# Kernel optimization log

Measured on AMD Instinct MI355X. Metric: run time of the kernel, lower is better.

Reference implementation:

```python
import jax, jax.numpy as jnp
import numpy as np

# Dimensions (Llama-3-8B-style GQA with paged KV cache)
B, S, HID = 1, 1024, 4096
H, HKV, D = 32, 8, 128
G = H // HKV
BLK = 16            # tokens per KV block
NB = 256            # blocks in storage
CB = 192            # context blocks attended (3072 tokens)
PAST = 2048         # tokens already cached before this step
NL = 2              # layers in kv_ptr
L = CB * BLK


def rotate_half(x):
    x1, x2 = x[..., : x.shape[-1] // 2], x[..., x.shape[-1] // 2:]
    return jnp.concatenate([-x2, x1], axis=-1)


def setup_inputs() -> dict:
    key = jax.random.key(0)
    ks = jax.random.split(key, 8)
    hidden_states = jax.random.normal(ks[0], (B, S, HID), jnp.float32)
    kv_ptr = jax.random.normal(ks[1], (NL, 2, NB, HKV, BLK, D), jnp.float32)
    Wq = 0.02 * jax.random.normal(ks[2], (H * D, HID), jnp.float32)
    Wk = 0.02 * jax.random.normal(ks[3], (HKV * D, HID), jnp.float32)
    Wv = 0.02 * jax.random.normal(ks[4], (HKV * D, HID), jnp.float32)
    Wo = 0.02 * jax.random.normal(ks[5], (HID, H * D), jnp.float32)
    # RoPE cache for the new tokens (global positions PAST..PAST+S-1), HF convention
    pos = (PAST + jnp.arange(S)).astype(jnp.float32)
    inv_freq = 1.0 / (10000.0 ** (jnp.arange(0, D, 2, dtype=jnp.float32) / D))
    freqs = pos[:, None] * inv_freq[None, :]                # [S, D/2]
    emb = jnp.concatenate([freqs, freqs], axis=-1)           # [S, D]
    cos = jnp.cos(emb)[None, None]                           # [1,1,S,D]
    sin = jnp.sin(emb)[None, None]
    new_q_lut = jnp.arange(S, dtype=jnp.int32)[None]         # identity query LUT
    new_kv_lut = (CB - S // BLK + jnp.arange(S // BLK, dtype=jnp.int32))[None]  # blocks 128..191
    all_kv_lut = jnp.arange(CB, dtype=jnp.int32)[None]       # blocks 0..191
    kv_pos = jnp.arange(L)
    q_pos = PAST + jnp.arange(S)
    mask = (kv_pos[None, None, :] <= q_pos[None, :, None])   # [1,S,L] causal over global positions
    cmd_groups = jnp.zeros((B, S), jnp.int32)                # split-K scheduling metadata (no math effect)
    return dict(hidden_states=hidden_states, kv_ptr=kv_ptr, new_q_lut=new_q_lut,
                new_kv_lut=new_kv_lut, all_kv_lut=all_kv_lut, mask=mask,
                cmd_groups=cmd_groups, cos=cos, sin=sin, Wq=Wq, Wk=Wk, Wv=Wv, Wo=Wo,
                layer_idx=0)


def reference(hidden_states, kv_ptr, new_q_lut, new_kv_lut, all_kv_lut, mask,
              cmd_groups, cos, sin, Wq, Wk, Wv, Wo, layer_idx):
    b, s, _ = hidden_states.shape
    # QKV projections (no bias)
    q = jnp.einsum('bsh,oh->bso', hidden_states, Wq).reshape(b, s, H, D).transpose(0, 2, 1, 3)
    k = jnp.einsum('bsh,oh->bso', hidden_states, Wk).reshape(b, s, HKV, D).transpose(0, 2, 1, 3)
    v = jnp.einsum('bsh,oh->bso', hidden_states, Wv).reshape(b, s, HKV, D).transpose(0, 2, 1, 3)
    # RoPE
    q = q * cos + rotate_half(q) * sin
    k = k * cos + rotate_half(k) * sin
    # fill_kv_block_storage: scatter new K/V blocks into this layer's storage (b == 1)
    kb = jnp.transpose(k[0].reshape(HKV, s // BLK, BLK, D), (1, 0, 2, 3))  # [nblk,HKV,BLK,D]
    vb = jnp.transpose(v[0].reshape(HKV, s // BLK, BLK, D), (1, 0, 2, 3))
    sk = kv_ptr[layer_idx, 0].at[new_kv_lut[0]].set(kb)
    sv = kv_ptr[layer_idx, 1].at[new_kv_lut[0]].set(vb)
    # qkv_attention: gather context blocks via LUT, masked GQA attention
    ck = jnp.transpose(sk[all_kv_lut[0]], (1, 0, 2, 3)).reshape(HKV, L, D)  # [HKV,L,D]
    cv = jnp.transpose(sv[all_kv_lut[0]], (1, 0, 2, 3)).reshape(HKV, L, D)
    qg = q[:, :, new_q_lut[0], :].reshape(b, HKV, G, s, D)
    scores = jnp.einsum('bkgsd,kld->bkgsl', qg, ck) / jnp.sqrt(jnp.float32(D))
    scores = jnp.where(mask[:, None, None], scores, jnp.finfo(scores.dtype).min)
    p = jax.nn.softmax(scores, axis=-1)
    o = jnp.einsum('bkgsl,kld->bkgsd', p, cv).reshape(b, H, s, D)
    o = o.transpose(0, 2, 1, 3).reshape(b, s, H * D)
    return jnp.einsum('bso,ho->bsh', o, Wo)
```

## Files before the change

### kernel.cpp

```cpp
#include <hip/hip_runtime.h>
#include <cstdint>
#include <cstddef>


typedef _Float16 f16;
typedef f16 f16x8 __attribute__((ext_vector_type(8)));
typedef f16 f16x4 __attribute__((ext_vector_type(4)));
typedef float f32x4 __attribute__((ext_vector_type(4)));

#define HIDN 4096
#define LCTX 3072
#define PASTN 2048
#define QK_SCALE_LOG2 0.12753102734366334f
#define RESC_THR 11.54f

__device__ __forceinline__ f32x4 mfma16(f16x8 a, f16x8 b, f32x4 c) {
    return __builtin_amdgcn_mfma_f32_16x16x32_f16(a, b, c, 0, 0, 0);
}
__device__ __forceinline__ f32x4 mfma16k16(f16x4 a, f16x4 b, f32x4 c) {
    return __builtin_amdgcn_mfma_f32_16x16x16f16(a, b, c, 0, 0, 0);
}

__device__ __forceinline__ void gl_lds16(const void* g, void* l) {
    auto gp = (const __attribute__((address_space(1))) unsigned int*)(uintptr_t)g;
    auto lp = (__attribute__((address_space(3))) unsigned int*)(uintptr_t)l;
    __builtin_amdgcn_global_load_lds(gp, lp, 16, 0, 0);
}

__device__ __forceinline__ uint32_t lds_lo(const void* p) {
    return (uint32_t)(uintptr_t)p;
}

#define TRRD(dst, va, OFF) \
    asm volatile("ds_read_b64_tr_b16 %0, %1 offset:" #OFF : "=v"(dst) : "v"(va))
#define WAITL(N) \
    asm volatile("s_waitcnt lgkmcnt(" #N ")" ::: "memory"); \
    __builtin_amdgcn_sched_barrier(0)

__global__ void cvt_all(const float* __restrict__ hidden, const float* __restrict__ Wq,
                        const float* __restrict__ Wk, const float* __restrict__ Wv,
                        f16* __restrict__ h16, f16* __restrict__ w16)
{
    int i = blockIdx.x * 256 + threadIdx.x;
    const float* src; f16* dst; int off;
    if (i < 1048576)      { src = hidden; dst = h16; off = i; }
    else if (i < 5242880) { src = Wq; dst = w16; off = i - 1048576; }
    else if (i < 6291456) { src = Wk; dst = w16 + (size_t)4096 * 4096; off = i - 5242880; }
    else                  { src = Wv; dst = w16 + (size_t)5120 * 4096; off = i - 6291456; }
    f32x4 v = *(const f32x4*)(src + (size_t)off * 4);
    f16x4 h;
#pragma unroll
    for (int j = 0; j < 4; j++) h[j] = (f16)v[j];
    *(f16x4*)(dst + (size_t)off * 4) = h;
}

template <int EPI>
__global__ __launch_bounds__(256, 3) void gemm_f16(
    const f16* __restrict__ A, const f16* __restrict__ B,
    float* __restrict__ Cf, f16* __restrict__ Cq, f16* __restrict__ Ck,
    f16* __restrict__ Cv, int M, int N, int K)
{
    __shared__ f16 As[128 * 64];
    __shared__ f16 Bs[128 * 64];

    const int t = threadIdx.x, lane = t & 63, w = t >> 6;
    const int wm = w >> 1, wn = w & 1;
    const int l16 = lane & 15, g16 = lane >> 4;
    const int m0 = blockIdx.y * 128, n0 = blockIdx.x * 128;

    const int srow = lane >> 3;
    const int sgr  = (lane & 7) ^ srow;

    const size_t aoff = (size_t)(m0 + w * 32 + srow) * K + sgr * 8;
    const size_t boff = (size_t)(n0 + w * 32 + srow) * K + sgr * 8;

    f32x4 acc[4][4];
#pragma unroll
    for (int i = 0; i < 4; i++)
#pragma unroll
        for (int j = 0; j < 4; j++) acc[i][j] = (f32x4){0.f, 0.f, 0.f, 0.f};

    for (int k0 = 0; k0 < K; k0 += 64) {
#pragma unroll
        for (int j = 0; j < 4; j++) {
            gl_lds16(A + aoff + (size_t)j * 8 * K + k0, (void*)(As + (w * 32 + j * 8) * 64));
            gl_lds16(B + boff + (size_t)j * 8 * K + k0, (void*)(Bs + (w * 32 + j * 8) * 64));
        }
        __syncthreads();

#pragma unroll
        for (int ks = 0; ks < 2; ks++) {
            f16x8 af[4], bfr[4];
#pragma unroll
            for (int mi = 0; mi < 4; mi++) {
                int r = wm * 64 + mi * 16 + l16;
                int g = ks * 4 + g16;
                af[mi] = *(const f16x8*)&As[r * 64 + ((g ^ (r & 7)) << 3)];
            }
#pragma unroll
            for (int ni = 0; ni < 4; ni++) {
                int r = wn * 64 + ni * 16 + l16;
                int g = ks * 4 + g16;
                bfr[ni] = *(const f16x8*)&Bs[r * 64 + ((g ^ (r & 7)) << 3)];
            }
#pragma unroll
            for (int ni = 0; ni < 4; ni++)
#pragma unroll
                for (int mi = 0; mi < 4; mi++)
                    acc[mi][ni] = mfma16(af[mi], bfr[ni], acc[mi][ni]);
        }
        __syncthreads();
    }

#pragma unroll
    for (int mi = 0; mi < 4; mi++)
#pragma unroll
        for (int ni = 0; ni < 4; ni++)
#pragma unroll
            for (int r = 0; r < 4; r++) {
                int row = m0 + wm * 64 + mi * 16 + (g16 << 2) + r;
                int col = n0 + wn * 64 + ni * 16 + l16;
                float val = acc[mi][ni][r];
                if (EPI == 0) {
                    if (col < 4096) {
                        Cq[(size_t)row * 4096 + col] = (f16)val;
                    } else if (col < 5120) {
                        Ck[(size_t)row * 1024 + (col - 4096)] = (f16)val;
                    } else {
                        int c = col - 5120;
                        int hh = c >> 7, d = c & 127;
                        Cv[((size_t)hh * LCTX + PASTN + row) * 128 + d] = (f16)val;
                    }
                } else {
                    Cf[(size_t)row * N + col] = val;
                }
            }
}

__global__ void aux_all(const float* __restrict__ Wo, f16* __restrict__ w16,
                        f16* __restrict__ q16, const f16* __restrict__ kraw,
                        const float* __restrict__ cosp, const float* __restrict__ sinp,
                        f16* __restrict__ ck, const float* __restrict__ kvp,
                        const int* __restrict__ layer, f16* __restrict__ cv)
{
    int i = blockIdx.x * 256 + threadIdx.x;
    if (i < 4194304) {
        f32x4 v = *(const f32x4*)(Wo + (size_t)i * 4);
        f16x4 h;
#pragma unroll
        for (int j = 0; j < 4; j++) h[j] = (f16)v[j];
        *(f16x4*)(w16 + (size_t)i * 4) = h;
    } else if (i < 4456448) {
        int ii = i - 4194304;
        int gd = ii & 7, hh = (ii >> 3) & 31, s = ii >> 8;
        size_t b1 = (size_t)s * 4096 + hh * 128 + gd * 8;
        f16x8 x1 = *(f16x8*)(q16 + b1);
        f16x8 x2 = *(f16x8*)(q16 + b1 + 64);
        const float* c1 = cosp + s * 128 + gd * 8;
        const float* s1 = sinp + s * 128 + gd * 8;
        f16x8 o1, o2;
#pragma unroll
        for (int j = 0; j < 8; j++) {
            float a = (float)x1[j], b = (float)x2[j];
            o1[j] = (f16)((a * c1[j] - b * s1[j]) * QK_SCALE_LOG2);
            o2[j] = (f16)((b * c1[j + 64] + a * s1[j + 64]) * QK_SCALE_LOG2);
        }
        *(f16x8*)(q16 + b1) = o1;
        *(f16x8*)(q16 + b1 + 64) = o2;
    } else if (i < 4521984) {
        int ii = i - 4456448;
        int gd = ii & 7, kvh = (ii >> 3) & 7, s = ii >> 6;
        size_t b1 = (size_t)s * 1024 + kvh * 128 + gd * 8;
        f16x8 x1 = *(const f16x8*)(kraw + b1);
        f16x8 x2 = *(const f16x8*)(kraw + b1 + 64);
        const float* c1 = cosp + s * 128 + gd * 8;
        const float* s1 = sinp + s * 128 + gd * 8;
        f16x8 o1, o2;
#pragma unroll
        for (int j = 0; j < 8; j++) {
            float a = (float)x1[j], b = (float)x2[j];
            o1[j] = (f16)(a * c1[j] - b * s1[j]);
            o2[j] = (f16)(b * c1[j + 64] + a * s1[j + 64]);
        }
        size_t dst = ((size_t)kvh * LCTX + PASTN + s) * 128 + gd * 8;
        *(f16x8*)(ck + dst) = o1;
        *(f16x8*)(ck + dst + 64) = o2;
    } else {
        int i4 = i - 4521984;
        int half = i4 >> 19;
        int e = (i4 & 524287) * 4;
        int hh = e >> 18, rem = e & 262143, l = rem >> 7, d = rem & 127;
        int blk = l >> 4, rr = l & 15;
        size_t src = (((size_t)(layer[0] * 2 + half) * 256 + blk) * 8 + hh) * 2048
                   + (size_t)rr * 128 + d;
        f32x4 x = *(const f32x4*)(kvp + src);
        f16x4 h;
#pragma unroll
        for (int j = 0; j < 4; j++) h[j] = (f16)x[j];
        size_t dst = ((size_t)hh * LCTX + l) * 128 + d;
        *(f16x4*)((half ? cv : ck) + dst) = h;
    }
}

__global__ __launch_bounds__(256, 2) void attn_part(
    const f16* __restrict__ Q, const f16* __restrict__ Kc,
    const f16* __restrict__ Vc, f16* __restrict__ Op, float* __restrict__ mlb)
{
    const int b = blockIdx.x;
    const int z = b >> 8;
    const int idx = b & 255;
    const int h = idx & 31;
    const int jj = idx >> 5;
    const int j = z ? (7 - jj) : jj;
    const int s0 = j * 128;
    const int kvh = h >> 2;
    const int t = threadIdx.x, lane = t & 63, w = t >> 6;
    const int l16 = lane & 15, g16 = lane >> 4;

    __shared__ f16 Ks[2][64 * 128];
    __shared__ f16 Vs[2][64 * 128];

    f16x8 qfA[4], qfB[4];
    {
        size_t baseA = (size_t)(s0 + w * 32 + l16) * 4096 + h * 128;
        size_t baseB = baseA + (size_t)16 * 4096;
#pragma unroll
        for (int kk = 0; kk < 4; kk++) {
            qfA[kk] = *(const f16x8*)(Q + baseA + kk * 32 + g16 * 8);
            qfB[kk] = *(const f16x8*)(Q + baseB + kk * 32 + g16 * 8);
        }
    }

    f32x4 ofA[8], ofB[8];
#pragma unroll
    for (int cf = 0; cf < 8; cf++) {
        ofA[cf] = (f32x4){0.f, 0.f, 0.f, 0.f};
        ofB[cf] = (f32x4){0.f, 0.f, 0.f, 0.f};
    }
    float mrA = -3.0e38f, lrA = 0.f;
    float mrB = -3.0e38f, lrB = 0.f;

    const f16* Kb = Kc + (size_t)kvh * LCTX * 128;
    const f16* Vb = Vc + (size_t)kvh * LCTX * 128;
    const int ntt = (PASTN + s0 + 128) >> 6;

    const int krow = lane >> 4;
    const int kp   = lane & 15;
    const int vrow = ((lane >> 5) << 4) + (((lane >> 3) & 3) << 2) + ((lane >> 1) & 3);
    const int vch  = (lane & 1) << 3;

    const uint32_t vs0 = lds_lo(Vs[0]) + lane * 8;
    const uint32_t vs1 = lds_lo(Vs[1]) + lane * 8;

#define STAGE_KV(l0, buf)                                                     \
    {                                                                         \
        _Pragma("unroll")                                                     \
        for (int jx = 0; jx < 4; jx++) {                                      \
            int r7 = ((jx & 1) << 2) + krow;                                  \
            int sg = kp ^ r7;                                                 \
            gl_lds16(Kb + (size_t)((l0) + w * 16 + jx * 4 + krow) * 128 + sg * 8, \
                     (void*)(Ks[buf] + (w * 16 + jx * 4) * 128));             \
        }                                                                     \
        _Pragma("unroll")                                                     \
        for (int q = 0; q < 4; q++) {                                         \
            gl_lds16(Vb + (size_t)((l0) + (q & 1) * 32 + vrow) * 128          \
                        + (w * 2 + (q >> 1)) * 16 + vch,                      \
                     (void*)(Vs[buf] + (w * 4 + q) * 512));                   \
        }                                                                     \
    }

    STAGE_KV(z * 64, 0);
    __syncthreads();

    int itp = 0;
    for (int it = z; it < ntt; it += 2, ++itp) {
        const int l0 = it << 6;
        const int cur = itp & 1;

        if (it + 2 < ntt) STAGE_KV(l0 + 128, cur ^ 1);

        f32x4 sA[4], sB[4];
#pragma unroll
        for (int ni = 0; ni < 4; ni++) {
            sA[ni] = (f32x4){0.f, 0.f, 0.f, 0.f};
            sB[ni] = (f32x4){0.f, 0.f, 0.f, 0.f};
        }
        __builtin_amdgcn_s_setprio(1);
#pragma unroll
        for (int ni = 0; ni < 4; ni++)
#pragma unroll
            for (int kk = 0; kk < 4; kk++) {
                int r = ni * 16 + l16;
                int g = kk * 4 + g16;
                f16x8 kh = *(const f16x8*)&Ks[cur][r * 128 + ((g ^ (r & 7)) << 3)];
                sA[ni] = mfma16(kh, qfA[kk], sA[ni]);
                sB[ni] = mfma16(kh, qfB[kk], sB[ni]);
            }
        __builtin_amdgcn_s_setprio(0);

#define SOFTMAX(sf, mr, lr, of, QOFF)                                          \
        {                                                                      \
            const int qrow = s0 + w * 32 + (QOFF) + l16;                       \
            if (l0 + 63 > PASTN + s0 + w * 32 + (QOFF)) {                      \
                _Pragma("unroll")                                              \
                for (int ni = 0; ni < 4; ni++)                                 \
                    _Pragma("unroll")                                          \
                    for (int r = 0; r < 4; r++) {                              \
                        int col = l0 + ni * 16 + (g16 << 2) + r;               \
                        if (col > PASTN + qrow) sf[ni][r] = -3.0e38f;          \
                    }                                                          \
            }                                                                  \
            float mx;                                                          \
            {                                                                  \
                f32x4 m4 = sf[0];                                              \
                _Pragma("unroll")                                              \
                for (int ni = 1; ni < 4; ni++) {                               \
                    m4[0] = fmaxf(m4[0], sf[ni][0]);                           \
                    m4[1] = fmaxf(m4[1], sf[ni][1]);                           \
                    m4[2] = fmaxf(m4[2], sf[ni][2]);                           \
                    m4[3] = fmaxf(m4[3], sf[ni][3]);                           \
                }                                                              \
                mx = fmaxf(fmaxf(m4[0], m4[1]), fmaxf(m4[2], m4[3]));          \
            }                                                                  \
            mx = fmaxf(mx, __shfl_xor(mx, 16));                                \
            mx = fmaxf(mx, __shfl_xor(mx, 32));                                \
            if (__any(mx > mr + RESC_THR)) {                                   \
                float mnew = fmaxf(mr, mx);                                    \
                float corr = exp2f(mr - mnew);                                 \
                mr = mnew;                                                     \
                lr *= corr;                                                    \
                float cr[4];                                                   \
                _Pragma("unroll")                                              \
                for (int r = 0; r < 4; r++) cr[r] = __shfl(corr, (g16 << 2) + r); \
                _Pragma("unroll")                                              \
                for (int cf = 0; cf < 8; cf++)                                 \
                    _Pragma("unroll")                                          \
                    for (int r = 0; r < 4; r++) of[cf][r] *= cr[r];            \
            }                                                                  \
            _Pragma("unroll")                                                  \
            for (int ni = 0; ni < 4; ni++)                                     \
                _Pragma("unroll")                                              \
                for (int r = 0; r < 4; r++) {                                  \
                    float p = exp2f(sf[ni][r] - mr);                           \
                    sf[ni][r] = p;                                             \
                    lr += p;                                                   \
                }                                                              \
        }

        SOFTMAX(sA, mrA, lrA, ofA, 0)
        SOFTMAX(sB, mrB, lrB, ofB, 16)

        f16x4 paA[4], paB[4];
#pragma unroll
        for (int ni = 0; ni < 4; ni++) {
            paA[ni][0] = (f16)sA[ni][0]; paA[ni][1] = (f16)sA[ni][1];
            paA[ni][2] = (f16)sA[ni][2]; paA[ni][3] = (f16)sA[ni][3];
            paB[ni][0] = (f16)sB[ni][0]; paB[ni][1] = (f16)sB[ni][1];
            paB[ni][2] = (f16)sB[ni][2]; paB[ni][3] = (f16)sB[ni][3];
        }

        {
            const uint32_t va = cur ? vs1 : vs0;
            f16x4 ra0, ra1, ra2, ra3, rb0, rb1, rb2, rb3;
            f16x4 rc0, rc1, rc2, rc3, rd0, rd1, rd2, rd3;
            __builtin_amdgcn_s_setprio(1);
            TRRD(ra0,va,0);     TRRD(ra1,va,512);   TRRD(ra2,va,1024);  TRRD(ra3,va,1536);
            TRRD(rb0,va,2048);  TRRD(rb1,va,2560);  TRRD(rb2,va,3072);  TRRD(rb3,va,3584);
            TRRD(rc0,va,4096);  TRRD(rc1,va,4608);  TRRD(rc2,va,5120);  TRRD(rc3,va,5632);
#define X2(cf, ni, reg) \
            ofA[cf] = mfma16k16(paA[ni], reg, ofA[cf]); \
            ofB[cf] = mfma16k16(paB[ni], reg, ofB[cf]);
            WAITL(8);
            X2(0,0,ra0) X2(0,1,ra1) X2(0,2,ra2) X2(0,3,ra3)
            TRRD(rd0,va,6144);  TRRD(rd1,va,6656);  TRRD(rd2,va,7168);  TRRD(rd3,va,7680);
            WAITL(8);
            X2(1,0,rb0) X2(1,1,rb1) X2(1,2,rb2) X2(1,3,rb3)
            TRRD(ra0,va,8192);  TRRD(ra1,va,8704);  TRRD(ra2,va,9216);  TRRD(ra3,va,9728);
            WAITL(8);
            X2(2,0,rc0) X2(2,1,rc1) X2(2,2,rc2) X2(2,3,rc3)
            TRRD(rb0,va,10240); TRRD(rb1,va,10752); TRRD(rb2,va,11264); TRRD(rb3,va,11776);
            WAITL(8);
            X2(3,0,rd0) X2(3,1,rd1) X2(3,2,rd2) X2(3,3,rd3)
            TRRD(rc0,va,12288); TRRD(rc1,va,12800); TRRD(rc2,va,13312); TRRD(rc3,va,13824);
            WAITL(8);
            X2(4,0,ra0) X2(4,1,ra1) X2(4,2,ra2) X2(4,3,ra3)
            TRRD(rd0,va,14336); TRRD(rd1,va,14848); TRRD(rd2,va,15360); TRRD(rd3,va,15872);
            WAITL(8);
            X2(5,0,rb0) X2(5,1,rb1) X2(5,2,rb2) X2(5,3,rb3)
            WAITL(4);
            X2(6,0,rc0) X2(6,1,rc1) X2(6,2,rc2) X2(6,3,rc3)
            WAITL(0);
            X2(7,0,rd0) X2(7,1,rd1) X2(7,2,rd2) X2(7,3,rd3)
#undef X2
            __builtin_amdgcn_s_setprio(0);
        }
        __syncthreads();
    }

#define WRITE_P(of, mr, lr, QOFF)                                             \
    {                                                                         \
        float l2 = lr + __shfl_xor(lr, 16);                                   \
        l2 += __shfl_xor(l2, 32);                                             \
        if (lane < 16) {                                                      \
            int srow = s0 + w * 32 + (QOFF) + lane;                           \
            *(float2*)(mlb + (((size_t)z * 1024 + srow) * 32 + h) * 2) =      \
                make_float2(mr, l2);                                          \
        }                                                                     \
        float lrr[4];                                                         \
        _Pragma("unroll")                                                     \
        for (int r = 0; r < 4; r++) lrr[r] = __shfl(l2, (g16 << 2) + r);      \
        _Pragma("unroll")                                                     \
        for (int cf = 0; cf < 8; cf++)                                        \
            _Pragma("unroll")                                                 \
            for (int r = 0; r < 4; r++) {                                     \
                int srow = s0 + w * 32 + (QOFF) + (g16 << 2) + r;             \
                int d = cf * 16 + l16;                                        \
                Op[(size_t)z * 4194304 + (size_t)srow * 4096                  \
                   + (size_t)h * 128 + d] = (f16)(of[cf][r] / lrr[r]);        \
            }                                                                 \
    }
    WRITE_P(ofA, mrA, lrA, 0)
    WRITE_P(ofB, mrB, lrB, 16)
#undef WRITE_P
#undef SOFTMAX
#undef STAGE_KV
}

__global__ void attn_combine(const f16* __restrict__ Op, const float* __restrict__ mlb,
                             f16* __restrict__ obuf)
{
    int i = blockIdx.x * 256 + threadIdx.x;
    int d8 = i & 15, hh = (i >> 4) & 31, s = i >> 9;
    float2 ml0 = *(const float2*)(mlb + (((size_t)0 * 1024 + s) * 32 + hh) * 2);
    float2 ml1 = *(const float2*)(mlb + (((size_t)1 * 1024 + s) * 32 + hh) * 2);
    float mstar = fmaxf(ml0.x, ml1.x);
    float w0 = exp2f(ml0.x - mstar) * ml0.y;
    float w1 = exp2f(ml1.x - mstar) * ml1.y;
    float inv = 1.0f / (w0 + w1);
    size_t off = (size_t)s * 4096 + (size_t)hh * 128 + d8 * 8;
    f16x8 a = *(const f16x8*)(Op + off);
    f16x8 b = *(const f16x8*)(Op + 4194304 + off);
    f16x8 o;
#pragma unroll
    for (int jx = 0; jx < 8; jx++)
        o[jx] = (f16)(((float)a[jx] * w0 + (float)b[jx] * w1) * inv);
    *(f16x8*)(obuf + off) = o;
}

extern "C" void kernel_launch(void* const* d_in, const int* in_sizes, int n_in,
                              void* d_out, int out_size, void* d_ws, size_t ws_size,
                              hipStream_t stream)
{
    const float* hidden = (const float*)d_in[0];
    const float* kvp    = (const float*)d_in[1];
    const float* cosp   = (const float*)d_in[7];
    const float* sinp   = (const float*)d_in[8];
    const float* Wq     = (const float*)d_in[9];
    const float* Wk     = (const float*)d_in[10];
    const float* Wv     = (const float*)d_in[11];
    const float* Wo     = (const float*)d_in[12];
    const int*   layer  = (const int*)d_in[13];

    char* ws = (char*)d_ws;
    f16* w16  = (f16*)ws;
    f16* opart= (f16*)(ws + 33554432);
    f16* h16  = (f16*)(ws + 50331648);
    f16* ck   = (f16*)(ws + 58720256);
    f16* cv   = (f16*)(ws + 65011712);
    f16* obuf = (f16*)(ws + 71303168);

    f16*   q16  = (f16*)d_out;
    f16*   kraw = (f16*)((char*)d_out + 8388608);
    float* mlb  = (float*)((char*)d_out + 8388608);

    cvt_all<<<28672, 256, 0, stream>>>(hidden, Wq, Wk, Wv, h16, w16);

    gemm_f16<0><<<dim3(48, 8), 256, 0, stream>>>(
        h16, w16, nullptr, q16, kraw, cv, 1024, 6144, 4096);

    aux_all<<<21760, 256, 0, stream>>>(Wo, w16, q16, kraw, cosp, sinp,
                                       ck, kvp, layer, cv);

    attn_part<<<dim3(512), 256, 0, stream>>>(q16, ck, cv, opart, mlb);

    attn_combine<<<2048, 256, 0, stream>>>(opart, mlb, obuf);

    gemm_f16<1><<<dim3(32, 8), 256, 0, stream>>>(
        obuf, w16, (float*)d_out, nullptr, nullptr, nullptr, 1024, 4096, 4096);
}
```

Measured before the change: 272.2 us.

## Fold KV-cache conversion into QKV GEMM blocks and compute softmax row sums via MFMA

The fp32-to-fp16 conversion of the cached K/V context moves out of the aux kernel into 256 extra blocks of the QKV GEMM launch (now a 1D grid), so it runs alongside the GEMM tiles. The attention kernel now accumulates softmax denominators with an extra MFMA against a ones vector instead of scalar adds and cross-lane shuffles. The m and l statistics are stored in separate arrays. Tradeoffs: extra MFMA work per tile, and the copy blocks compete with GEMM blocks for CUs. Row sums now come from fp16-rounded probabilities.

```diff
diff --git a/kernel.cpp b/kernel.cpp
--- a/kernel.cpp
+++ b/kernel.cpp
@@ -58,15 +58,42 @@
 __global__ __launch_bounds__(256, 3) void gemm_f16(
     const f16* __restrict__ A, const f16* __restrict__ B,
     float* __restrict__ Cf, f16* __restrict__ Cq, f16* __restrict__ Ck,
-    f16* __restrict__ Cv, int M, int N, int K)
+    f16* __restrict__ Cv, int M, int N, int K,
+    const float* __restrict__ kvp, const int* __restrict__ layer,
+    f16* __restrict__ ckc)
 {
     __shared__ f16 As[128 * 64];
     __shared__ f16 Bs[128 * 64];
 
+    const int bx = blockIdx.x;
+
+    if (EPI == 0 && bx >= 384) {
+        const int lay = layer[0];
+        int base = (bx - 384) * 256 + threadIdx.x;
+#pragma unroll
+        for (int pass = 0; pass < 16; ++pass) {
+            int i4 = base + pass * 65536;
+            int half = i4 >> 19;
+            int e = (i4 & 524287) * 4;
+            int hh = e >> 18, rem = e & 262143, l = rem >> 7, d = rem & 127;
+            int blk = l >> 4, rr = l & 15;
+            size_t src = (((size_t)(lay * 2 + half) * 256 + blk) * 8 + hh) * 2048
+                       + (size_t)rr * 128 + d;
+            f32x4 x = *(const f32x4*)(kvp + src);
+            f16x4 h;
+#pragma unroll
+            for (int j = 0; j < 4; j++) h[j] = (f16)x[j];
+            size_t dst = ((size_t)hh * LCTX + l) * 128 + d;
+            *(f16x4*)((half ? Cv : ckc) + dst) = h;
+        }
+        return;
+    }
+
     const int t = threadIdx.x, lane = t & 63, w = t >> 6;
     const int wm = w >> 1, wn = w & 1;
     const int l16 = lane & 15, g16 = lane >> 4;
-    const int m0 = blockIdx.y * 128, n0 = blockIdx.x * 128;
+    const int nx = (EPI == 0) ? 48 : 32;
+    const int m0 = (bx / nx) * 128, n0 = (bx % nx) * 128;
 
     const int srow = lane >> 3;
     const int sgr  = (lane & 7) ^ srow;
@@ -137,11 +164,10 @@
             }
 }
 
-__global__ void aux_all(const float* __restrict__ Wo, f16* __restrict__ w16,
-                        f16* __restrict__ q16, const f16* __restrict__ kraw,
-                        const float* __restrict__ cosp, const float* __restrict__ sinp,
-                        f16* __restrict__ ck, const float* __restrict__ kvp,
-                        const int* __restrict__ layer, f16* __restrict__ cv)
+__global__ void aux2(const float* __restrict__ Wo, f16* __restrict__ w16,
+                     f16* __restrict__ q16, const f16* __restrict__ kraw,
+                     const float* __restrict__ cosp, const float* __restrict__ sinp,
+                     f16* __restrict__ ck)
 {
     int i = blockIdx.x * 256 + threadIdx.x;
     if (i < 4194304) {
@@ -167,7 +193,7 @@
         }
         *(f16x8*)(q16 + b1) = o1;
         *(f16x8*)(q16 + b1 + 64) = o2;
-    } else if (i < 4521984) {
+    } else {
         int ii = i - 4456448;
         int gd = ii & 7, kvh = (ii >> 3) & 7, s = ii >> 6;
         size_t b1 = (size_t)s * 1024 + kvh * 128 + gd * 8;
@@ -185,26 +211,13 @@
         size_t dst = ((size_t)kvh * LCTX + PASTN + s) * 128 + gd * 8;
         *(f16x8*)(ck + dst) = o1;
         *(f16x8*)(ck + dst + 64) = o2;
-    } else {
-        int i4 = i - 4521984;
-        int half = i4 >> 19;
-        int e = (i4 & 524287) * 4;
-        int hh = e >> 18, rem = e & 262143, l = rem >> 7, d = rem & 127;
-        int blk = l >> 4, rr = l & 15;
-        size_t src = (((size_t)(layer[0] * 2 + half) * 256 + blk) * 8 + hh) * 2048
-                   + (size_t)rr * 128 + d;
-        f32x4 x = *(const f32x4*)(kvp + src);
-        f16x4 h;
-#pragma unroll
-        for (int j = 0; j < 4; j++) h[j] = (f16)x[j];
-        size_t dst = ((size_t)hh * LCTX + l) * 128 + d;
-        *(f16x4*)((half ? cv : ck) + dst) = h;
     }
 }
 
 __global__ __launch_bounds__(256, 2) void attn_part(
     const f16* __restrict__ Q, const f16* __restrict__ Kc,
-    const f16* __restrict__ Vc, f16* __restrict__ Op, float* __restrict__ mlb)
+    const f16* __restrict__ Vc, f16* __restrict__ Op,
+    float* __restrict__ mlb_m, float* __restrict__ mlb_l)
 {
     const int b = blockIdx.x;
     const int z = b >> 8;
@@ -237,8 +250,10 @@
         ofA[cf] = (f32x4){0.f, 0.f, 0.f, 0.f};
         ofB[cf] = (f32x4){0.f, 0.f, 0.f, 0.f};
     }
-    float mrA = -3.0e38f, lrA = 0.f;
-    float mrB = -3.0e38f, lrB = 0.f;
+    f32x4 lsA = (f32x4){0.f, 0.f, 0.f, 0.f};
+    f32x4 lsB = (f32x4){0.f, 0.f, 0.f, 0.f};
+    float mrA = -3.0e38f, mrB = -3.0e38f;
+    const f16x4 vone = {(f16)1.f, (f16)1.f, (f16)1.f, (f16)1.f};
 
     const f16* Kb = Kc + (size_t)kvh * LCTX * 128;
     const f16* Vb = Vc + (size_t)kvh * LCTX * 128;
@@ -298,7 +313,7 @@
             }
         __builtin_amdgcn_s_setprio(0);
 
-#define SOFTMAX(sf, mr, lr, of, QOFF)                                          \
+#define SOFTMAX(sf, mr, ls, of, QOFF)                                          \
         {                                                                      \
             const int qrow = s0 + w * 32 + (QOFF) + l16;                       \
             if (l0 + 63 > PASTN + s0 + w * 32 + (QOFF)) {                      \
@@ -328,10 +343,11 @@
                 float mnew = fmaxf(mr, mx);                                    \
                 float corr = exp2f(mr - mnew);                                 \
                 mr = mnew;                                                     \
-                lr *= corr;                                                    \
                 float cr[4];                                                   \
                 _Pragma("unroll")                                              \
                 for (int r = 0; r < 4; r++) cr[r] = __shfl(corr, (g16 << 2) + r); \
+                _Pragma("unroll")                                              \
+                for (int r = 0; r < 4; r++) ls[r] *= cr[r];                    \
                 _Pragma("unroll")                                              \
                 for (int cf = 0; cf < 8; cf++)                                 \
                     _Pragma("unroll")                                          \
@@ -340,15 +356,12 @@
             _Pragma("unroll")                                                  \
             for (int ni = 0; ni < 4; ni++)                                     \
                 _Pragma("unroll")                                              \
-                for (int r = 0; r < 4; r++) {                                  \
-                    float p = exp2f(sf[ni][r] - mr);                           \
-                    sf[ni][r] = p;                                             \
-                    lr += p;                                                   \
-                }                                                              \
-        }
-
-        SOFTMAX(sA, mrA, lrA, ofA, 0)
-        SOFTMAX(sB, mrB, lrB, ofB, 16)
+                for (int r = 0; r < 4; r++)                                    \
+                    sf[ni][r] = exp2f(sf[ni][r] - mr);                         \
+        }
+
+        SOFTMAX(sA, mrA, lsA, ofA, 0)
+        SOFTMAX(sB, mrB, lsB, ofB, 16)
 
         f16x4 paA[4], paB[4];
 #pragma unroll
@@ -367,6 +380,11 @@
             TRRD(ra0,va,0);     TRRD(ra1,va,512);   TRRD(ra2,va,1024);  TRRD(ra3,va,1536);
             TRRD(rb0,va,2048);  TRRD(rb1,va,2560);  TRRD(rb2,va,3072);  TRRD(rb3,va,3584);
             TRRD(rc0,va,4096);  TRRD(rc1,va,4608);  TRRD(rc2,va,5120);  TRRD(rc3,va,5632);
+#pragma unroll
+            for (int ni = 0; ni < 4; ni++) {
+                lsA = mfma16k16(paA[ni], vone, lsA);
+                lsB = mfma16k16(paB[ni], vone, lsB);
+            }
 #define X2(cf, ni, reg) \
             ofA[cf] = mfma16k16(paA[ni], reg, ofA[cf]); \
             ofB[cf] = mfma16k16(paB[ni], reg, ofB[cf]);
@@ -397,18 +415,19 @@
         __syncthreads();
     }
 
-#define WRITE_P(of, mr, lr, QOFF)                                             \
+#define WRITE_P(of, mr, ls, QOFF)                                             \
     {                                                                         \
-        float l2 = lr + __shfl_xor(lr, 16);                                   \
-        l2 += __shfl_xor(l2, 32);                                             \
         if (lane < 16) {                                                      \
             int srow = s0 + w * 32 + (QOFF) + lane;                           \
-            *(float2*)(mlb + (((size_t)z * 1024 + srow) * 32 + h) * 2) =      \
-                make_float2(mr, l2);                                          \
+            mlb_m[((size_t)z * 1024 + srow) * 32 + h] = mr;                   \
         }                                                                     \
-        float lrr[4];                                                         \
-        _Pragma("unroll")                                                     \
-        for (int r = 0; r < 4; r++) lrr[r] = __shfl(l2, (g16 << 2) + r);      \
+        if (l16 == 0) {                                                       \
+            _Pragma("unroll")                                                 \
+            for (int r = 0; r < 4; r++) {                                     \
+                int srow = s0 + w * 32 + (QOFF) + (g16 << 2) + r;             \
+                mlb_l[((size_t)z * 1024 + srow) * 32 + h] = ls[r];            \
+            }                                                                 \
+        }                                                                     \
         _Pragma("unroll")                                                     \
         for (int cf = 0; cf < 8; cf++)                                        \
             _Pragma("unroll")                                                 \
@@ -416,26 +435,30 @@
                 int srow = s0 + w * 32 + (QOFF) + (g16 << 2) + r;             \
                 int d = cf * 16 + l16;                                        \
                 Op[(size_t)z * 4194304 + (size_t)srow * 4096                  \
-                   + (size_t)h * 128 + d] = (f16)(of[cf][r] / lrr[r]);        \
+                   + (size_t)h * 128 + d] = (f16)(of[cf][r] / ls[r]);         \
             }                                                                 \
     }
-    WRITE_P(ofA, mrA, lrA, 0)
-    WRITE_P(ofB, mrB, lrB, 16)
+    WRITE_P(ofA, mrA, lsA, 0)
+    WRITE_P(ofB, mrB, lsB, 16)
 #undef WRITE_P
 #undef SOFTMAX
 #undef STAGE_KV
 }
 
-__global__ void attn_combine(const f16* __restrict__ Op, const float* __restrict__ mlb,
+__global__ void attn_combine(const f16* __restrict__ Op,
+                             const float* __restrict__ mlb_m,
+                             const float* __restrict__ mlb_l,
                              f16* __restrict__ obuf)
 {
     int i = blockIdx.x * 256 + threadIdx.x;
     int d8 = i & 15, hh = (i >> 4) & 31, s = i >> 9;
-    float2 ml0 = *(const float2*)(mlb + (((size_t)0 * 1024 + s) * 32 + hh) * 2);
-    float2 ml1 = *(const float2*)(mlb + (((size_t)1 * 1024 + s) * 32 + hh) * 2);
-    float mstar = fmaxf(ml0.x, ml1.x);
-    float w0 = exp2f(ml0.x - mstar) * ml0.y;
-    float w1 = exp2f(ml1.x - mstar) * ml1.y;
+    float m0 = mlb_m[(size_t)s * 32 + hh];
+    float m1 = mlb_m[(size_t)(1024 + s) * 32 + hh];
+    float l0 = mlb_l[(size_t)s * 32 + hh];
+    float l1 = mlb_l[(size_t)(1024 + s) * 32 + hh];
+    float mstar = fmaxf(m0, m1);
+    float w0 = exp2f(m0 - mstar) * l0;
+    float w1 = exp2f(m1 - mstar) * l1;
     float inv = 1.0f / (w0 + w1);
     size_t off = (size_t)s * 4096 + (size_t)hh * 128 + d8 * 8;
     f16x8 a = *(const f16x8*)(Op + off);
@@ -469,22 +492,23 @@
     f16* cv   = (f16*)(ws + 65011712);
     f16* obuf = (f16*)(ws + 71303168);
 
-    f16*   q16  = (f16*)d_out;
-    f16*   kraw = (f16*)((char*)d_out + 8388608);
-    float* mlb  = (float*)((char*)d_out + 8388608);
+    f16*   q16   = (f16*)d_out;
+    f16*   kraw  = (f16*)((char*)d_out + 8388608);
+    float* mlb_m = (float*)((char*)d_out + 8388608);
+    float* mlb_l = (float*)((char*)d_out + 8650752);
 
     cvt_all<<<28672, 256, 0, stream>>>(hidden, Wq, Wk, Wv, h16, w16);
 
-    gemm_f16<0><<<dim3(48, 8), 256, 0, stream>>>(
-        h16, w16, nullptr, q16, kraw, cv, 1024, 6144, 4096);
-
-    aux_all<<<21760, 256, 0, stream>>>(Wo, w16, q16, kraw, cosp, sinp,
-                                       ck, kvp, layer, cv);
-
-    attn_part<<<dim3(512), 256, 0, stream>>>(q16, ck, cv, opart, mlb);
-
-    attn_combine<<<2048, 256, 0, stream>>>(opart, mlb, obuf);
-
-    gemm_f16<1><<<dim3(32, 8), 256, 0, stream>>>(
-        obuf, w16, (float*)d_out, nullptr, nullptr, nullptr, 1024, 4096, 4096);
-}
+    gemm_f16<0><<<dim3(640), 256, 0, stream>>>(
+        h16, w16, nullptr, q16, kraw, cv, 1024, 6144, 4096, kvp, layer, ck);
+
+    aux2<<<17664, 256, 0, stream>>>(Wo, w16, q16, kraw, cosp, sinp, ck);
+
+    attn_part<<<dim3(512), 256, 0, stream>>>(q16, ck, cv, opart, mlb_m, mlb_l);
+
+    attn_combine<<<2048, 256, 0, stream>>>(opart, mlb_m, mlb_l, obuf);
+
+    gemm_f16<1><<<dim3(256), 256, 0, stream>>>(
+        obuf, w16, (float*)d_out, nullptr, nullptr, nullptr, 1024, 4096, 4096,
+        nullptr, nullptr, nullptr);
+}
```

Result: no change. 275.3 us (+1.1%).

## Fold KV cache conversion into QKV GEMM tail blocks; halve O-proj tile height

Applied to the files above, without the earlier changes.

The QKV projection GEMM now launches 512 blocks on a 1D grid. The first 384 compute GEMM tiles and the last 128 convert the cached fp32 K/V blocks to fp16, a job taken out of the aux kernel. This lets the memory-bound cache conversion overlap with the compute-bound GEMM instead of running as a separate phase. The output projection GEMM is templated to a 64-row tile, doubling its block count to 512 so more CUs are filled, at the cost of less reuse per tile.

```diff
diff --git a/kernel.cpp b/kernel.cpp
--- a/kernel.cpp
+++ b/kernel.cpp
@@ -54,46 +54,79 @@
     *(f16x4*)(dst + (size_t)off * 4) = h;
 }
 
-template <int EPI>
+template <int EPI, int BM>
 __global__ __launch_bounds__(256, 3) void gemm_f16(
     const f16* __restrict__ A, const f16* __restrict__ B,
     float* __restrict__ Cf, f16* __restrict__ Cq, f16* __restrict__ Ck,
-    f16* __restrict__ Cv, int M, int N, int K)
+    f16* __restrict__ Cv, int M, int N, int K,
+    const float* __restrict__ kvp, const int* __restrict__ layer,
+    f16* __restrict__ ckc)
 {
-    __shared__ f16 As[128 * 64];
+    __shared__ f16 As[BM * 64];
     __shared__ f16 Bs[128 * 64];
+
+    const int bx = blockIdx.x;
+
+    if (EPI == 0 && bx >= 384) {
+        const int lay = layer[0];
+        int base = (bx - 384) * 256 + threadIdx.x;
+#pragma unroll
+        for (int pass = 0; pass < 32; ++pass) {
+            int i4 = base + pass * 32768;
+            int half = i4 >> 19;
+            int e = (i4 & 524287) * 4;
+            int hh = e >> 18, rem = e & 262143, l = rem >> 7, d = rem & 127;
+            int blk = l >> 4, rr = l & 15;
+            size_t src = (((size_t)(lay * 2 + half) * 256 + blk) * 8 + hh) * 2048
+                       + (size_t)rr * 128 + d;
+            f32x4 x = *(const f32x4*)(kvp + src);
+            f16x4 h;
+#pragma unroll
+            for (int j = 0; j < 4; j++) h[j] = (f16)x[j];
+            size_t dst = ((size_t)hh * LCTX + l) * 128 + d;
+            *(f16x4*)((half ? Cv : ckc) + dst) = h;
+        }
+        return;
+    }
+
+    constexpr int RPW = BM / 4;
+    constexpr int MI  = BM / 32;
 
     const int t = threadIdx.x, lane = t & 63, w = t >> 6;
     const int wm = w >> 1, wn = w & 1;
     const int l16 = lane & 15, g16 = lane >> 4;
-    const int m0 = blockIdx.y * 128, n0 = blockIdx.x * 128;
+    const int nx = (EPI == 0) ? 48 : 32;
+    const int m0 = (bx / nx) * BM, n0 = (bx % nx) * 128;
 
     const int srow = lane >> 3;
     const int sgr  = (lane & 7) ^ srow;
 
-    const size_t aoff = (size_t)(m0 + w * 32 + srow) * K + sgr * 8;
+    const size_t aoff = (size_t)(m0 + w * RPW + srow) * K + sgr * 8;
     const size_t boff = (size_t)(n0 + w * 32 + srow) * K + sgr * 8;
 
-    f32x4 acc[4][4];
-#pragma unroll
-    for (int i = 0; i < 4; i++)
+    f32x4 acc[MI][4];
+#pragma unroll
+    for (int i = 0; i < MI; i++)
 #pragma unroll
         for (int j = 0; j < 4; j++) acc[i][j] = (f32x4){0.f, 0.f, 0.f, 0.f};
 
     for (int k0 = 0; k0 < K; k0 += 64) {
 #pragma unroll
-        for (int j = 0; j < 4; j++) {
-            gl_lds16(A + aoff + (size_t)j * 8 * K + k0, (void*)(As + (w * 32 + j * 8) * 64));
-            gl_lds16(B + boff + (size_t)j * 8 * K + k0, (void*)(Bs + (w * 32 + j * 8) * 64));
-        }
+        for (int j = 0; j < RPW / 8; j++)
+            gl_lds16(A + aoff + (size_t)j * 8 * K + k0,
+                     (void*)(As + (w * RPW + j * 8) * 64));
+#pragma unroll
+        for (int j = 0; j < 4; j++)
+            gl_lds16(B + boff + (size_t)j * 8 * K + k0,
+                     (void*)(Bs + (w * 32 + j * 8) * 64));
         __syncthreads();
 
 #pragma unroll
         for (int ks = 0; ks < 2; ks++) {
-            f16x8 af[4], bfr[4];
-#pragma unroll
-            for (int mi = 0; mi < 4; mi++) {
-                int r = wm * 64 + mi * 16 + l16;
+            f16x8 af[MI], bfr[4];
+#pragma unroll
+            for (int mi = 0; mi < MI; mi++) {
+                int r = wm * (BM / 2) + mi * 16 + l16;
                 int g = ks * 4 + g16;
                 af[mi] = *(const f16x8*)&As[r * 64 + ((g ^ (r & 7)) << 3)];
             }
@@ -106,19 +139,19 @@
 #pragma unroll
             for (int ni = 0; ni < 4; ni++)
 #pragma unroll
-                for (int mi = 0; mi < 4; mi++)
+                for (int mi = 0; mi < MI; mi++)
                     acc[mi][ni] = mfma16(af[mi], bfr[ni], acc[mi][ni]);
         }
         __syncthreads();
     }
 
 #pragma unroll
-    for (int mi = 0; mi < 4; mi++)
+    for (int mi = 0; mi < MI; mi++)
 #pragma unroll
         for (int ni = 0; ni < 4; ni++)
 #pragma unroll
             for (int r = 0; r < 4; r++) {
-                int row = m0 + wm * 64 + mi * 16 + (g16 << 2) + r;
+                int row = m0 + wm * (BM / 2) + mi * 16 + (g16 << 2) + r;
                 int col = n0 + wn * 64 + ni * 16 + l16;
                 float val = acc[mi][ni][r];
                 if (EPI == 0) {
@@ -137,11 +170,10 @@
             }
 }
 
-__global__ void aux_all(const float* __restrict__ Wo, f16* __restrict__ w16,
-                        f16* __restrict__ q16, const f16* __restrict__ kraw,
-                        const float* __restrict__ cosp, const float* __restrict__ sinp,
-                        f16* __restrict__ ck, const float* __restrict__ kvp,
-                        const int* __restrict__ layer, f16* __restrict__ cv)
+__global__ void aux2(const float* __restrict__ Wo, f16* __restrict__ w16,
+                     f16* __restrict__ q16, const f16* __restrict__ kraw,
+                     const float* __restrict__ cosp, const float* __restrict__ sinp,
+                     f16* __restrict__ ck)
 {
     int i = blockIdx.x * 256 + threadIdx.x;
     if (i < 4194304) {
@@ -167,7 +199,7 @@
         }
         *(f16x8*)(q16 + b1) = o1;
         *(f16x8*)(q16 + b1 + 64) = o2;
-    } else if (i < 4521984) {
+    } else {
         int ii = i - 4456448;
         int gd = ii & 7, kvh = (ii >> 3) & 7, s = ii >> 6;
         size_t b1 = (size_t)s * 1024 + kvh * 128 + gd * 8;
@@ -185,20 +217,6 @@
         size_t dst = ((size_t)kvh * LCTX + PASTN + s) * 128 + gd * 8;
         *(f16x8*)(ck + dst) = o1;
         *(f16x8*)(ck + dst + 64) = o2;
-    } else {
-        int i4 = i - 4521984;
-        int half = i4 >> 19;
-        int e = (i4 & 524287) * 4;
-        int hh = e >> 18, rem = e & 262143, l = rem >> 7, d = rem & 127;
-        int blk = l >> 4, rr = l & 15;
-        size_t src = (((size_t)(layer[0] * 2 + half) * 256 + blk) * 8 + hh) * 2048
-                   + (size_t)rr * 128 + d;
-        f32x4 x = *(const f32x4*)(kvp + src);
-        f16x4 h;
-#pragma unroll
-        for (int j = 0; j < 4; j++) h[j] = (f16)x[j];
-        size_t dst = ((size_t)hh * LCTX + l) * 128 + d;
-        *(f16x4*)((half ? cv : ck) + dst) = h;
     }
 }
 
@@ -475,16 +493,16 @@
 
     cvt_all<<<28672, 256, 0, stream>>>(hidden, Wq, Wk, Wv, h16, w16);
 
-    gemm_f16<0><<<dim3(48, 8), 256, 0, stream>>>(
-        h16, w16, nullptr, q16, kraw, cv, 1024, 6144, 4096);
-
-    aux_all<<<21760, 256, 0, stream>>>(Wo, w16, q16, kraw, cosp, sinp,
-                                       ck, kvp, layer, cv);
+    gemm_f16<0, 128><<<dim3(512), 256, 0, stream>>>(
+        h16, w16, nullptr, q16, kraw, cv, 1024, 6144, 4096, kvp, layer, ck);
+
+    aux2<<<17664, 256, 0, stream>>>(Wo, w16, q16, kraw, cosp, sinp, ck);
 
     attn_part<<<dim3(512), 256, 0, stream>>>(q16, ck, cv, opart, mlb);
 
     attn_combine<<<2048, 256, 0, stream>>>(opart, mlb, obuf);
 
-    gemm_f16<1><<<dim3(32, 8), 256, 0, stream>>>(
-        obuf, w16, (float*)d_out, nullptr, nullptr, nullptr, 1024, 4096, 4096);
-}
+    gemm_f16<1, 64><<<dim3(512), 256, 0, stream>>>(
+        obuf, w16, (float*)d_out, nullptr, nullptr, nullptr, 1024, 4096, 4096,
+        nullptr, nullptr, nullptr);
+}
```

Result: no change. 274.0 us (+0.7%).
